# Optimization experiments

Measured on AMD Instinct MI355X. Metric: run time of the kernel, lower is better.

Reference implementation:

```python
import jax, jax.numpy as jnp
import numpy as np

RADIUS = 0.4
NSAMPLE = 32
NORMALIZE_DP = True


def setup_inputs() -> dict:
    key = jax.random.key(0)
    k1, k2, k3 = jax.random.split(key, 3)
    B, N, K, C = 2, 16384, 4096, 128
    xyz = jax.random.normal(k1, (B, N, 3), dtype=jnp.float32)
    new_xyz = jax.random.normal(k2, (B, K, 3), dtype=jnp.float32)
    features = jax.random.normal(k3, (B, C, N), dtype=jnp.float32)
    return {"xyz": xyz, "new_xyz": new_xyz, "features": features}


def _ball_query(radius, nsample, xyz, new_xyz):
    # xyz: (B,N,3), new_xyz: (B,K,3) -> indices (B,K,nsample) int32
    N = xyz.shape[1]
    # squared distances via ||a||^2 + ||b||^2 - 2 a.b  -> (B,K,N)
    d2 = (jnp.sum(new_xyz * new_xyz, -1)[:, :, None]
          + jnp.sum(xyz * xyz, -1)[:, None, :]
          - 2.0 * jnp.einsum('bkd,bnd->bkn', new_xyz, xyz))
    mask = d2 < radius * radius
    # key = point index if inside ball else N (sentinel); take nsample smallest
    key = jnp.where(mask, jnp.arange(N, dtype=jnp.int32), jnp.int32(N))
    neg_top, _ = jax.lax.top_k(-key, nsample)  # (B,K,nsample)
    idx = -neg_top
    # pointnet2 semantics: pad with first in-radius index (0 if ball empty)
    first = idx[..., :1]
    first = jnp.where(first < N, first, 0)
    idx = jnp.where(idx < N, idx, first)
    return idx


def _group(features, idx):
    # features: (B,C,N), idx: (B,K,ns) -> (B,C,K,ns)
    return jax.vmap(lambda f, i: f[:, i])(features, idx)


def reference(xyz, new_xyz, features):
    idx = _ball_query(RADIUS, NSAMPLE, xyz, new_xyz)          # (B,K,ns)
    xyz_t = jnp.transpose(xyz, (0, 2, 1))                      # (B,3,N)
    grouped_xyz = _group(xyz_t, idx)                           # (B,3,K,ns)
    grouped_xyz = grouped_xyz - jnp.transpose(new_xyz, (0, 2, 1))[..., None]
    if NORMALIZE_DP:
        grouped_xyz = grouped_xyz / RADIUS
    grouped_features = _group(features, idx)                   # (B,C,K,ns)
    return (grouped_xyz, grouped_features)
```

## Files before the change

kernel.cpp:

```cpp
#include <hip/hip_runtime.h>

#define BB 2
#define NN 16384
#define KK 4096
#define CC 128
#define SS 32

typedef float vfloat4 __attribute__((ext_vector_type(4)));

__global__ __launch_bounds__(256) void transpose_prep_kernel(
    const float* __restrict__ feat, const float* __restrict__ xyz,
    float* __restrict__ feat_t, float* __restrict__ xyzw)
{
    __shared__ float tile[64][133];
    const int b  = blockIdx.x >> 8;
    const int n0 = (blockIdx.x & 255) * 64;
    const int t  = threadIdx.x;

    if (t < 64) {
        const int i = b * NN + n0 + t;
        const float* p = xyz + (size_t)i * 3;
        const float x = p[0], y = p[1], z = p[2];
        const float pp = __fadd_rn(__fadd_rn(__fmul_rn(x, x), __fmul_rn(y, y)),
                                   __fmul_rn(z, z));
        vfloat4 v = {x, y, z, pp};
        *(vfloat4*)(xyzw + (size_t)i * 4) = v;
    }

    const int ln = t & 63;
    const int cr = t >> 6;
#pragma unroll
    for (int p = 0; p < 32; ++p) {
        const int c = p * 4 + cr;
        tile[ln][c] = feat[((size_t)b * CC + c) * NN + n0 + ln];
    }
    __syncthreads();

    const int cl = t & 31;
    const int ns = t >> 5;
#pragma unroll
    for (int p = 0; p < 8; ++p) {
        const int n = ns + 8 * p;
        float* dst = feat_t + ((size_t)(b * NN + n0 + n)) * CC;
#pragma unroll
        for (int j = 0; j < 4; ++j)
            dst[cl + 32 * j] = tile[n][cl + 32 * j];
    }
}

__global__ __launch_bounds__(256) void ball_query_kernel(
    const float* __restrict__ xyzw,
    const float* __restrict__ new_xyz,
    int* __restrict__ idx_buf)
{
    const int wave = threadIdx.x >> 6;
    const int lane = threadIdx.x & 63;
    const int qi   = blockIdx.x * 4 + wave;
    const int b    = qi >> 12;
    const int k    = qi & (KK - 1);

    const float R2 = (float)(0.4 * 0.4);

    const float* q = new_xyz + (size_t)(b * KK + k) * 3;
    const float qx = q[0], qy = q[1], qz = q[2];
    const float qq = __fadd_rn(__fadd_rn(__fmul_rn(qx, qx), __fmul_rn(qy, qy)),
                               __fmul_rn(qz, qz));

    const vfloat4* xw = (const vfloat4*)xyzw + (size_t)b * NN;
    int* out = idx_buf + (size_t)qi * SS;

    int cnt = 0;
    int first = -1;

    auto process = [&](int base, vfloat4 v) {
        const float dot = __fadd_rn(__fadd_rn(__fmul_rn(qx, v.x), __fmul_rn(qy, v.y)),
                                    __fmul_rn(qz, v.z));
        const float d2 = __fsub_rn(__fadd_rn(qq, v.w), __fmul_rn(2.0f, dot));
        const bool inball = d2 < R2;
        const unsigned long long mask = __ballot(inball);
        if (mask) {
            if (first < 0) first = base + (int)__builtin_ctzll(mask);
            if (inball) {
                const int pos = cnt + __popcll(mask & ((1ull << lane) - 1ull));
                if (pos < SS) out[pos] = base + lane;
            }
            cnt += __popcll(mask);
        }
    };

    vfloat4 v0 = xw[lane];
    vfloat4 v1 = xw[64 + lane];
    vfloat4 v2 = xw[128 + lane];
    vfloat4 v3 = xw[192 + lane];

    for (int base = 0; base < NN; base += 256) {
        const int nb = (base + 256 < NN) ? base + 256 : 0;
        vfloat4 u0 = xw[nb + lane];
        vfloat4 u1 = xw[nb + 64 + lane];
        vfloat4 u2 = xw[nb + 128 + lane];
        vfloat4 u3 = xw[nb + 192 + lane];

        process(base, v0);
        process(base + 64, v1);
        process(base + 128, v2);
        process(base + 192, v3);
        if (cnt >= SS) break;

        v0 = u0; v1 = u1; v2 = u2; v3 = u3;
    }

    const int fill = (first < 0) ? 0 : first;
    if (lane < SS && lane >= cnt) out[lane] = fill;
}

__global__ __launch_bounds__(256) void group_kernel(
    const float* __restrict__ xyzw,
    const float* __restrict__ new_xyz,
    const float* __restrict__ feat_t,
    const int*   __restrict__ idx_buf,
    float* __restrict__ out)
{
    __shared__ int   lidx[SS];
    __shared__ float tile[SS][132];
    __shared__ float txyz[3][SS];

    const int t  = threadIdx.x;
    const int bk = blockIdx.x;
    const int b  = bk >> 12;
    const int k  = bk & (KK - 1);

    if (t < SS) lidx[t] = idx_buf[(size_t)bk * SS + t];
    __syncthreads();

    const int cl = t & 31;
    const int sg = t >> 5;
#pragma unroll
    for (int p = 0; p < 4; ++p) {
        const int s = sg + 8 * p;
        const int n = lidx[s];
        const vfloat4 v = *(const vfloat4*)(feat_t + ((size_t)(b * NN + n)) * CC + 4 * cl);
        *(vfloat4*)&tile[s][4 * cl] = v;
    }

    if (t < SS) {
        const float* q = new_xyz + (size_t)bk * 3;
        const vfloat4 w = *((const vfloat4*)xyzw + (size_t)b * NN + lidx[t]);
        txyz[0][t] = (w.x - q[0]) / 0.4f;
        txyz[1][t] = (w.y - q[1]) / 0.4f;
        txyz[2][t] = (w.z - q[2]) / 0.4f;
    }
    __syncthreads();

    float* out_xyz  = out;
    float* out_feat = out + (size_t)BB * 3 * KK * SS;

    const int sq = t & 7;
    const int c0 = t >> 3;
#pragma unroll
    for (int p = 0; p < 4; ++p) {
        const int c = c0 + 32 * p;
        vfloat4 v;
        v.x = tile[4 * sq + 0][c];
        v.y = tile[4 * sq + 1][c];
        v.z = tile[4 * sq + 2][c];
        v.w = tile[4 * sq + 3][c];
        __builtin_nontemporal_store(
            v, (vfloat4*)(out_feat + (((size_t)(b * CC + c) * KK + k) * SS + 4 * sq)));
    }

    if (t < 24) {
        const int d   = t >> 3;
        const int sq2 = t & 7;
        const vfloat4 v = *(vfloat4*)&txyz[d][4 * sq2];
        __builtin_nontemporal_store(
            v, (vfloat4*)(out_xyz + (((size_t)(b * 3 + d) * KK + k) * SS + 4 * sq2)));
    }
}

extern "C" void kernel_launch(void* const* d_in, const int* in_sizes, int n_in,
                              void* d_out, int out_size, void* d_ws, size_t ws_size,
                              hipStream_t stream) {
    const float* xyz     = (const float*)d_in[0];
    const float* new_xyz = (const float*)d_in[1];
    const float* feat    = (const float*)d_in[2];
    float* out = (float*)d_out;

    int*   idx_buf = (int*)d_ws;
    float* xyzw    = (float*)((char*)d_ws + (1 << 20));
    float* feat_t  = (float*)((char*)d_ws + (1 << 20) + (512 << 10));

    transpose_prep_kernel<<<dim3(BB * (NN / 64)), dim3(256), 0, stream>>>(
        feat, xyz, feat_t, xyzw);

    ball_query_kernel<<<dim3(BB * KK / 4), dim3(256), 0, stream>>>(
        xyzw, new_xyz, idx_buf);

    group_kernel<<<dim3(BB * KK), dim3(256), 0, stream>>>(
        xyzw, new_xyz, feat_t, idx_buf, out);
}
```

Measured before the change: 90.79 us.

## Gather features directly into LDS with XOR-swizzled layout in group kernel

The group kernel now uses global_load_lds to copy gathered feature rows straight into shared memory, skipping the register round-trip. It drops the shared index staging and its barrier, with each lane reading its index from global memory. An XOR swizzle on 16-byte chunks replaces the padded tile to avoid LDS bank conflicts on the transposed reads. The direct-to-LDS path depends on the instruction's per-wave contiguous placement matching the swizzle math, which adds correctness risk.

```diff
diff --git a/kernel.cpp b/kernel.cpp
--- a/kernel.cpp
+++ b/kernel.cpp
@@ -120,35 +120,40 @@
     const int*   __restrict__ idx_buf,
     float* __restrict__ out)
 {
-    __shared__ int   lidx[SS];
-    __shared__ float tile[SS][132];
+    __shared__ float tile[SS * CC];
     __shared__ float txyz[3][SS];
 
-    const int t  = threadIdx.x;
-    const int bk = blockIdx.x;
-    const int b  = bk >> 12;
-    const int k  = bk & (KK - 1);
-
-    if (t < SS) lidx[t] = idx_buf[(size_t)bk * SS + t];
-    __syncthreads();
-
-    const int cl = t & 31;
-    const int sg = t >> 5;
+    const int t    = threadIdx.x;
+    const int l    = t & 63;
+    const int w    = t >> 6;
+    const int bk   = blockIdx.x;
+    const int b    = bk >> 12;
+    const int k    = bk & (KK - 1);
+    const int half = l >> 5;
+    const int cl   = l & 31;
+
 #pragma unroll
     for (int p = 0; p < 4; ++p) {
-        const int s = sg + 8 * p;
-        const int n = lidx[s];
-        const vfloat4 v = *(const vfloat4*)(feat_t + ((size_t)(b * NN + n)) * CC + 4 * cl);
-        *(vfloat4*)&tile[s][4 * cl] = v;
+        const int r = 8 * w + 2 * p;
+        const int s = r + half;
+        const int n = idx_buf[bk * SS + s];
+        const int chunk = cl ^ ((s >> 2) & 7);
+        const float* src = feat_t + ((size_t)(b * NN + n)) * CC + 4 * chunk;
+        __builtin_amdgcn_global_load_lds(
+            (const __attribute__((address_space(1))) void*)src,
+            (__attribute__((address_space(3))) void*)(tile + r * CC),
+            16, 0, 0);
     }
 
     if (t < SS) {
+        const int n = idx_buf[bk * SS + t];
         const float* q = new_xyz + (size_t)bk * 3;
-        const vfloat4 w = *((const vfloat4*)xyzw + (size_t)b * NN + lidx[t]);
-        txyz[0][t] = (w.x - q[0]) / 0.4f;
-        txyz[1][t] = (w.y - q[1]) / 0.4f;
-        txyz[2][t] = (w.z - q[2]) / 0.4f;
-    }
+        const vfloat4 wv = *((const vfloat4*)xyzw + (size_t)b * NN + n);
+        txyz[0][t] = (wv.x - q[0]) / 0.4f;
+        txyz[1][t] = (wv.y - q[1]) / 0.4f;
+        txyz[2][t] = (wv.z - q[2]) / 0.4f;
+    }
+
     __syncthreads();
 
     float* out_xyz  = out;
@@ -158,12 +163,13 @@
     const int c0 = t >> 3;
 #pragma unroll
     for (int p = 0; p < 4; ++p) {
-        const int c = c0 + 32 * p;
+        const int c  = c0 + 32 * p;
+        const int co = (((c >> 2) ^ sq) << 2) + (c & 3);
         vfloat4 v;
-        v.x = tile[4 * sq + 0][c];
-        v.y = tile[4 * sq + 1][c];
-        v.z = tile[4 * sq + 2][c];
-        v.w = tile[4 * sq + 3][c];
+        v.x = tile[(4 * sq + 0) * CC + co];
+        v.y = tile[(4 * sq + 1) * CC + co];
+        v.z = tile[(4 * sq + 2) * CC + co];
+        v.w = tile[(4 * sq + 3) * CC + co];
         __builtin_nontemporal_store(
             v, (vfloat4*)(out_feat + (((size_t)(b * CC + c) * KK + k) * SS + 4 * sq)));
     }
```

Result: no change. 91.08 us (+0.3%).
